# Kernel tuning notes

Measured on AMD Instinct MI355X. Metric: run time of the kernel, lower is better.

## Reference

```python
import jax, jax.numpy as jnp
import numpy as np

M, N, H, C = 32, 1024, 64, 10  # samples, nodes(==feature dim), hidden, classes
SLOPE = 0.2


def setup_inputs() -> dict:
    key = jax.random.key(0)
    ks = jax.random.split(key, 6)
    features = jax.random.normal(ks[0], (M, N, N), jnp.float32)           # [M, N, D], D == N
    weights = jax.random.uniform(ks[1], (M, N, N), jnp.float32)           # nonneg adjacency weights
    std = (2.0 / (1.0 + SLOPE ** 2) / N) ** 0.5                            # kaiming_normal for leaky_relu
    w_gnn0 = jax.random.normal(ks[2], (N, H), jnp.float32) * std
    w_gnn1 = jax.random.normal(ks[3], (N, H), jnp.float32) * std
    w_gnn2 = jax.random.normal(ks[4], (N, H), jnp.float32) * std
    fc_w = jax.random.normal(ks[5], (H, C), jnp.float32) * (1.0 / H ** 0.5)
    fc_b = jnp.zeros((C,), jnp.float32)
    return {
        "features": features,
        "weights": weights,
        "w_gnn0": w_gnn0,
        "w_gnn1": w_gnn1,
        "w_gnn2": w_gnn2,
        "fc_w": fc_w,
        "fc_b": fc_b,
        "view_flag": 0,
    }


def _forward(features, weights, w_gnn0, w_gnn1, w_gnn2, fc_w, fc_b, view_flag):
    Wg = (w_gnn0, w_gnn1, w_gnn2)[view_flag]  # static selection
    _, Nn, _ = features.shape
    Cc = fc_b.shape[0]
    eye = jnp.eye(Nn, dtype=features.dtype)
    rows = jnp.arange(Nn)

    def structural_enhancement(W, p):
        # Literal torch semantics: max_id is always 0 (scores_list[i] is 0-dim),
        # so rows i < p get column-0 entry set to 1 where > 0. Score/cos-sim
        # suppression never affects outputs (scores_list is discarded).
        col0 = W[:, 0]
        new_col0 = jnp.where((rows < p) & (col0 > 0), jnp.asarray(1.0, W.dtype), col0)
        return W.at[:, 0].set(new_col0)

    def per_sample(X, W0):
        XW = X @ Wg  # [N, H]; X and Wg are loop-invariant
        feat_s = jnp.zeros((Wg.shape[1],), X.dtype)
        sr_s = jnp.zeros((Cc,), X.dtype)
        b_s = jnp.zeros((Cc,), X.dtype)
        u_s = jnp.asarray(0.0, X.dtype)
        u0 = jnp.asarray(999.0, X.dtype)
        done = jnp.asarray(False)
        W = W0
        for t in range(1, 9):  # while-loop is bounded: break guaranteed at 5*t >= 40
            adjp = 0.5 * structural_enhancement(W, 5 * t) + eye  # [N, N]
            h = adjp @ XW                                         # [N, H]
            h = jnp.where(h >= 0, h, SLOPE * h)                   # leaky_relu (dropout p=0 / eval)
            feat = h.mean(axis=0)                                 # global avg pool over nodes -> [H]
            sr = jax.nn.softplus(feat @ fc_w + fc_b)              # [C]
            S = sr.sum() + Cc
            u = Cc / S
            brk = (u >= u0) | (5 * t >= 40)
            store = jnp.logical_and(~done, ~brk)
            W = jnp.where(store, adjp, W)
            u0 = jnp.where(store, u, u0)
            feat_s = jnp.where(store, feat, feat_s)
            sr_s = jnp.where(store, sr, sr_s)
            b_s = jnp.where(store, sr / S, b_s)
            u_s = jnp.where(store, u, u_s)
            done = jnp.logical_or(done, brk)
        return feat_s, W, sr_s, b_s, u_s

    return jax.vmap(per_sample)(features, weights)


def reference(features, weights, w_gnn0, w_gnn1, w_gnn2, fc_w, fc_b, view_flag):
    # returns (aft_feat [M,H], weights [M,N,N], single_results [M,C], bb [M,C], uu [M])
    return _forward(features, weights, w_gnn0, w_gnn1, w_gnn2, fc_w, fc_b, view_flag)
```

## Files before the change

kernel.cpp:

```cpp
#include <hip/hip_runtime.h>
#include <math.h>

#define MS 32
#define NN 1024
#define HH 64
#define CC 10
#define SLOPEF 0.2f

typedef __attribute__((ext_vector_type(8))) short bf16x8;
typedef __attribute__((ext_vector_type(4))) float f32x4;
typedef __attribute__((ext_vector_type(4))) unsigned int u32x4;

__device__ __forceinline__ void split2(float v, unsigned short& hi, unsigned short& lo) {
    unsigned u = __builtin_bit_cast(unsigned, v);
    hi = (unsigned short)(u >> 16);
    float hf = __builtin_bit_cast(float, u & 0xFFFF0000u);
    float l = v - hf;
    lo = (unsigned short)(__builtin_bit_cast(unsigned, l) >> 16);
}

__global__ __launch_bounds__(256) void split_B_sel(
    const float* __restrict__ B0, const float* __restrict__ B1,
    const float* __restrict__ B2, const int* __restrict__ flag,
    unsigned short* __restrict__ dh, unsigned short* __restrict__ dl)
{
    int vf = flag[0];
    const float* B = (vf == 0) ? B0 : (vf == 1 ? B1 : B2);
    int c = blockIdx.x;
    const float* src = B + (long)c * 64 * HH;
    unsigned short* dh_img = dh + (long)c * 4096;
    unsigned short* dl_img = dl + (long)c * 4096;

    __shared__ float tile[64][65];
    const int t = threadIdx.x;
    #pragma unroll
    for (int q = 0; q < 4; ++q) {
        int lin = q * 256 + t;
        int r = lin >> 4;
        int c4 = (lin & 15) << 2;
        float4 v = *reinterpret_cast<const float4*>(src + (long)r * HH + c4);
        tile[r][c4 + 0] = v.x; tile[r][c4 + 1] = v.y;
        tile[r][c4 + 2] = v.z; tile[r][c4 + 3] = v.w;
    }
    __syncthreads();
    const int col = t >> 2;
    const int seg = t & 3;
    unsigned short h8[16], l8[16];
    #pragma unroll
    for (int j = 0; j < 16; ++j)
        split2(tile[seg * 16 + j][col], h8[j], l8[j]);
    int base = col * 128 + seg * 32;
    int swz  = (col & 7) << 4;
    *reinterpret_cast<u32x4*>((char*)dh_img + ((base +  0) ^ swz)) = *reinterpret_cast<u32x4*>(h8);
    *reinterpret_cast<u32x4*>((char*)dh_img + ((base + 16) ^ swz)) = *reinterpret_cast<u32x4*>(h8 + 8);
    *reinterpret_cast<u32x4*>((char*)dl_img + ((base +  0) ^ swz)) = *reinterpret_cast<u32x4*>(l8);
    *reinterpret_cast<u32x4*>((char*)dl_img + ((base + 16) ^ swz)) = *reinterpret_cast<u32x4*>(l8 + 8);
}

template <int MODE>
__global__ __launch_bounds__(256, 4) void gemm_split(
    const float* __restrict__ A, long aStride,
    const unsigned short* __restrict__ Bh, const unsigned short* __restrict__ Bl,
    long bStrideH,
    const float* __restrict__ XWf,
    unsigned short* __restrict__ ChOut,
    unsigned short* __restrict__ ClOut,
    float* __restrict__ Cmat)
{
    __shared__ __align__(16) char smem[32768];
    unsigned short* Ahi = (unsigned short*)(smem);
    unsigned short* Alo = (unsigned short*)(smem + 8192);
    unsigned short* Bhi = (unsigned short*)(smem + 16384);
    unsigned short* Blo = (unsigned short*)(smem + 24576);

    const int m = blockIdx.y;
    const int row0 = blockIdx.x * 64;
    const float* A_m = A + (long)m * aStride + (long)row0 * NN;
    const u32x4* bh4 = reinterpret_cast<const u32x4*>(Bh + (bStrideH ? (long)m * bStrideH : 0L));
    const u32x4* bl4 = reinterpret_cast<const u32x4*>(Bl + (bStrideH ? (long)m * bStrideH : 0L));

    const int tid = threadIdx.x;
    const int w   = tid >> 6;
    const int l   = tid & 63;
    const int l15 = l & 15;
    const int lg  = l >> 4;

    f32x4 acc[4] = {};

    int lin_r[4], lin_c4[4];
    #pragma unroll
    for (int q = 0; q < 4; ++q) {
        int lin = q * 256 + tid;
        lin_r[q]  = lin >> 4;
        lin_c4[q] = (lin & 15) << 2;
    }

    f32x4 av[4];
    u32x4 bhreg[2], blreg[2];
    #pragma unroll
    for (int q = 0; q < 4; ++q) {
        const f32x4* p = reinterpret_cast<const f32x4*>(A_m + (long)lin_r[q] * NN + lin_c4[q]);
        av[q] = (MODE == 1) ? *p : __builtin_nontemporal_load(p);
    }
    bhreg[0] = bh4[tid];       bhreg[1] = bh4[256 + tid];
    blreg[0] = bl4[tid];       blreg[1] = bl4[256 + tid];

    for (int kc = 0; kc < 16; ++kc) {
        #pragma unroll
        for (int q = 0; q < 4; ++q) {
            ushort4 h, lw;
            split2(av[q].x, h.x, lw.x);
            split2(av[q].y, h.y, lw.y);
            split2(av[q].z, h.z, lw.z);
            split2(av[q].w, h.w, lw.w);
            int byte = (lin_r[q] * 128 + lin_c4[q] * 2) ^ ((lin_r[q] & 7) << 4);
            *reinterpret_cast<ushort4*>((char*)Ahi + byte) = h;
            *reinterpret_cast<ushort4*>((char*)Alo + byte) = lw;
        }
        reinterpret_cast<u32x4*>(Bhi)[tid]       = bhreg[0];
        reinterpret_cast<u32x4*>(Bhi)[256 + tid] = bhreg[1];
        reinterpret_cast<u32x4*>(Blo)[tid]       = blreg[0];
        reinterpret_cast<u32x4*>(Blo)[256 + tid] = blreg[1];
        __syncthreads();

        if (kc < 15) {
            int ko = (kc + 1) * 64;
            #pragma unroll
            for (int q = 0; q < 4; ++q) {
                const f32x4* p = reinterpret_cast<const f32x4*>(A_m + (long)lin_r[q] * NN + ko + lin_c4[q]);
                av[q] = (MODE == 1) ? *p : __builtin_nontemporal_load(p);
            }
            int cb = (kc + 1) * 512;
            bhreg[0] = bh4[cb + tid];       bhreg[1] = bh4[cb + 256 + tid];
            blreg[0] = bl4[cb + tid];       blreg[1] = bl4[cb + 256 + tid];
        }

        #pragma unroll
        for (int s = 0; s < 2; ++s) {
            int arow  = w * 16 + l15;
            int abyte = (arow * 128 + s * 64 + lg * 16) ^ ((arow & 7) << 4);
            bf16x8 ah = *reinterpret_cast<bf16x8*>((char*)Ahi + abyte);
            bf16x8 al = *reinterpret_cast<bf16x8*>((char*)Alo + abyte);
            #pragma unroll
            for (int fc = 0; fc < 4; ++fc) {
                int col   = fc * 16 + l15;
                int bbyte = (col * 128 + s * 64 + lg * 16) ^ ((col & 7) << 4);
                bf16x8 bh8 = *reinterpret_cast<bf16x8*>((char*)Bhi + bbyte);
                bf16x8 bl8 = *reinterpret_cast<bf16x8*>((char*)Blo + bbyte);
                acc[fc] = __builtin_amdgcn_mfma_f32_16x16x32_bf16(ah, bh8, acc[fc], 0, 0, 0);
                acc[fc] = __builtin_amdgcn_mfma_f32_16x16x32_bf16(ah, bl8, acc[fc], 0, 0, 0);
                acc[fc] = __builtin_amdgcn_mfma_f32_16x16x32_bf16(al, bh8, acc[fc], 0, 0, 0);
            }
        }
        __syncthreads();
    }

    if constexpr (MODE == 0) {
        float* C_m = Cmat + (long)m * NN * HH + (long)row0 * HH;
        unsigned short* dh = ChOut + (long)m * HH * NN + (long)blockIdx.x * 4096;
        unsigned short* dl = ClOut + (long)m * HH * NN + (long)blockIdx.x * 4096;
        const int kb = (w * 16 + lg * 4) * 2;
        #pragma unroll
        for (int fc = 0; fc < 4; ++fc) {
            int col = fc * 16 + l15;
            ushort4 h4, l4;
            split2(acc[fc][0], h4.x, l4.x);
            split2(acc[fc][1], h4.y, l4.y);
            split2(acc[fc][2], h4.z, l4.z);
            split2(acc[fc][3], h4.w, l4.w);
            #pragma unroll
            for (int r = 0; r < 4; ++r) {
                int row = w * 16 + lg * 4 + r;
                C_m[(long)row * HH + col] = acc[fc][r];
            }
            int byte = (col * 128 + kb) ^ ((col & 7) << 4);
            *reinterpret_cast<ushort4*>((char*)dh + byte) = h4;
            *reinterpret_cast<ushort4*>((char*)dl + byte) = l4;
        }
    } else {
        float* red2 = (float*)(smem);
        float* x0s  = (float*)(smem + 8192);
        const float* XWm = XWf + (long)m * NN * HH;
        if (tid < 64) x0s[tid] = XWm[tid];
        __syncthreads();

        int grows[4]; float v[4], bc[4];
        #pragma unroll
        for (int r = 0; r < 4; ++r) {
            int lrow = w * 16 + lg * 4 + r;
            grows[r] = row0 + lrow;
            v[r] = A[(long)m * aStride + (long)grows[r] * NN];
            bc[r] = 0.0f;
        }
        float xwv[4][4];
        #pragma unroll
        for (int fc = 0; fc < 4; ++fc) {
            int col = fc * 16 + l15;
            #pragma unroll
            for (int r = 0; r < 4; ++r)
                xwv[fc][r] = XWm[(long)grows[r] * HH + col];
        }

        float alpha = 1.0f, gamma = 0.0f;
        #pragma unroll
        for (int t = 1; t <= 8; ++t) {
            #pragma unroll
            for (int r = 0; r < 4; ++r) {
                float c = (grows[r] < 5 * t && v[r] > 0.0f) ? (1.0f - v[r]) : 0.0f;
                bc[r] = 0.5f * (bc[r] + c);
                v[r]  = 0.5f * (v[r] + c) + (grows[r] == 0 ? 1.0f : 0.0f);
            }
            alpha *= 0.5f;
            gamma = 0.5f * gamma + 1.0f;
            #pragma unroll
            for (int fc = 0; fc < 4; ++fc) {
                float x0c = x0s[fc * 16 + l15];
                float s = 0.0f;
                #pragma unroll
                for (int r = 0; r < 4; ++r) {
                    float y = alpha * acc[fc][r] + bc[r] * x0c + gamma * xwv[fc][r];
                    s += (y >= 0.0f) ? y : SLOPEF * y;
                }
                s += __shfl_xor(s, 16);
                s += __shfl_xor(s, 32);
                if (l < 16) red2[(w * 8 + (t - 1)) * 64 + fc * 16 + l] = s;
            }
        }
        __syncthreads();
        if (tid < 512) {
            int t8 = tid >> 6, col = tid & 63;
            float p = red2[(0 * 8 + t8) * 64 + col] + red2[(1 * 8 + t8) * 64 + col] +
                      red2[(2 * 8 + t8) * 64 + col] + red2[(3 * 8 + t8) * 64 + col];
            Cmat[(((long)m * 16 + blockIdx.x) * 8 + t8) * 64 + col] = p;
        }
    }
}

__global__ __launch_bounds__(512) void decide_kernel(
    const float* __restrict__ partials,
    const float* __restrict__ weights,
    const float* __restrict__ fc_w,
    const float* __restrict__ fc_b,
    float* __restrict__ col0k,
    int* __restrict__ k_arr,
    float* __restrict__ out_feat,
    float* __restrict__ out_sr,
    float* __restrict__ out_b,
    float* __restrict__ out_u)
{
    __shared__ float feat[8][64];
    __shared__ float sr_all[8][CC];
    __shared__ float Ss[8], us[8];
    __shared__ int ksh;

    const int m = blockIdx.x;
    const int tid = threadIdx.x;

    {
        int t8 = tid >> 6, col = tid & 63;
        float s = 0.0f;
        for (int bx = 0; bx < 16; ++bx)
            s += partials[(((long)m * 16 + bx) * 8 + t8) * 64 + col];
        feat[t8][col] = s * (1.0f / NN);
    }
    __syncthreads();

    if (tid < 80) {
        int t8 = tid / 10, c = tid % 10;
        float a = fc_b[c];
        for (int h = 0; h < HH; ++h) a += feat[t8][h] * fc_w[h * CC + c];
        sr_all[t8][c] = log1pf(expf(-fabsf(a))) + fmaxf(a, 0.0f);
    }
    __syncthreads();

    if (tid < 8) {
        float S = (float)CC;
        for (int c = 0; c < CC; ++c) S += sr_all[tid][c];
        Ss[tid] = S;
        us[tid] = (float)CC / S;
    }
    __syncthreads();

    if (tid == 0) {
        float u0 = 999.0f; int k = 1;
        for (int tt = 1; tt <= 8; ++tt) {
            float u = us[tt - 1];
            int brk = (u >= u0) || (tt == 8);
            if (!brk) { k = tt; u0 = u; } else break;
        }
        ksh = k;
        k_arr[m] = k;
        out_u[m] = us[k - 1];
    }
    __syncthreads();

    const int k = ksh;
    if (tid < 64) out_feat[m * HH + tid] = feat[k - 1][tid];
    if (tid < CC) {
        out_sr[m * CC + tid] = sr_all[k - 1][tid];
        out_b[m * CC + tid]  = sr_all[k - 1][tid] / Ss[k - 1];
    }
    for (int i = tid; i < NN; i += 512) {
        float v = weights[(long)m * NN * NN + (long)i * NN];
        for (int s = 1; s <= k; ++s) {
            float c = (i < 5 * s && v > 0.0f) ? (1.0f - v) : 0.0f;
            v = 0.5f * (v + c) + (i == 0 ? 1.0f : 0.0f);
        }
        col0k[m * NN + i] = v;
    }
}

__global__ __launch_bounds__(256) void finalize_W(
    const float* __restrict__ W0, const float* __restrict__ col0k,
    const int* __restrict__ k_arr, float* __restrict__ outW)
{
    const long n4 = (long)MS * NN * NN / 4;
    const long stride = (long)gridDim.x * 256;
    for (long i4 = (long)blockIdx.x * 256 + threadIdx.x; i4 < n4; i4 += stride) {
        long e = i4 * 4;
        int m = (int)(e >> 20);
        int i = (int)((e >> 10) & 1023);
        int j = (int)(e & 1023);
        int k = k_arr[m];
        float scale = 1.0f / (float)(1 << k);
        float diagadd = 2.0f * (1.0f - scale);

        f32x4 wv = reinterpret_cast<const f32x4*>(W0)[i4];
        float v0 = scale * wv.x + ((i == j + 0) ? diagadd : 0.0f);
        float v1 = scale * wv.y + ((i == j + 1) ? diagadd : 0.0f);
        float v2 = scale * wv.z + ((i == j + 2) ? diagadd : 0.0f);
        float v3 = scale * wv.w + ((i == j + 3) ? diagadd : 0.0f);
        if (j == 0) v0 = col0k[m * NN + i];
        f32x4 o = {v0, v1, v2, v3};
        __builtin_nontemporal_store(o, reinterpret_cast<f32x4*>(outW) + i4);
    }
}

extern "C" void kernel_launch(void* const* d_in, const int* in_sizes, int n_in,
                              void* d_out, int out_size, void* d_ws, size_t ws_size,
                              hipStream_t stream)
{
    const float* features = (const float*)d_in[0];
    const float* weights  = (const float*)d_in[1];
    const float* w_gnn0   = (const float*)d_in[2];
    const float* w_gnn1   = (const float*)d_in[3];
    const float* w_gnn2   = (const float*)d_in[4];
    const float* fc_w     = (const float*)d_in[5];
    const float* fc_b     = (const float*)d_in[6];
    const int*   viewFlag = (const int*)d_in[7];

    float* out = (float*)d_out;
    float* out_feat = out;
    float* outW     = out + (long)MS * HH;
    float* out_sr   = outW + (long)MS * NN * NN;
    float* out_b    = out_sr + MS * CC;
    float* out_u    = out_b + MS * CC;

    float* wsf = (float*)d_ws;
    float* XWf            = wsf;
    unsigned short* XWh   = (unsigned short*)(XWf + (long)MS * NN * HH);
    unsigned short* XWl   = XWh + (long)MS * HH * NN;
    unsigned short* Wgh   = XWl + (long)MS * HH * NN;
    unsigned short* Wgl   = Wgh + (long)HH * NN;
    float* partials       = (float*)(Wgl + (long)HH * NN);
    float* col0k          = partials + (long)MS * 16 * 8 * 64;
    int*   k_arr          = (int*)(col0k + (long)MS * NN);

    split_B_sel<<<16, 256, 0, stream>>>(w_gnn0, w_gnn1, w_gnn2, viewFlag, Wgh, Wgl);
    dim3 gemmGrid(NN / 64, MS);
    gemm_split<0><<<gemmGrid, 256, 0, stream>>>(features, (long)NN * NN,
                                                Wgh, Wgl, 0L, nullptr,
                                                XWh, XWl, XWf);
    gemm_split<1><<<gemmGrid, 256, 0, stream>>>(weights, (long)NN * NN,
                                                XWh, XWl, (long)HH * NN, XWf,
                                                nullptr, nullptr, partials);
    decide_kernel<<<MS, 512, 0, stream>>>(partials, weights, fc_w, fc_b,
                                          col0k, k_arr,
                                          out_feat, out_sr, out_b, out_u);
    finalize_W<<<2048, 256, 0, stream>>>(weights, col0k, k_arr, outW);
}
```

Baseline: 122.0 us.

## Fuse decide step into second GEMM via last-block counter, drop fp32 XW buffer

Moves the per-sample decision logic (feature pooling, classifier, softplus, break selection and column-0 update) into the tail of the second GEMM. The last block to finish for each sample, found through an atomic counter, runs that logic, which removes one kernel launch. The fp32 XW intermediate is no longer written; the second GEMM rebuilds the needed XW values from the bf16 hi/lo split buffers. This saves a 32x1024x64 float store plus its reload, at the cost of slightly different precision for those values and added threadfence/atomic synchronisation.

```diff
diff --git a/kernel.cpp b/kernel.cpp
--- a/kernel.cpp
+++ b/kernel.cpp
@@ -17,6 +17,10 @@
     float hf = __builtin_bit_cast(float, u & 0xFFFF0000u);
     float l = v - hf;
     lo = (unsigned short)(__builtin_bit_cast(unsigned, l) >> 16);
+}
+
+__device__ __forceinline__ float bf16_to_f32(unsigned short h) {
+    return __builtin_bit_cast(float, (unsigned)h << 16);
 }
 
 __global__ __launch_bounds__(256) void split_B_sel(
@@ -62,10 +66,18 @@
     const float* __restrict__ A, long aStride,
     const unsigned short* __restrict__ Bh, const unsigned short* __restrict__ Bl,
     long bStrideH,
-    const float* __restrict__ XWf,
     unsigned short* __restrict__ ChOut,
     unsigned short* __restrict__ ClOut,
-    float* __restrict__ Cmat)
+    float* __restrict__ partials,
+    int* __restrict__ counters,
+    const float* __restrict__ fc_w,
+    const float* __restrict__ fc_b,
+    float* __restrict__ col0k,
+    int* __restrict__ k_arr,
+    float* __restrict__ out_feat,
+    float* __restrict__ out_sr,
+    float* __restrict__ out_b,
+    float* __restrict__ out_u)
 {
     __shared__ __align__(16) char smem[32768];
     unsigned short* Ahi = (unsigned short*)(smem);
@@ -76,14 +88,19 @@
     const int m = blockIdx.y;
     const int row0 = blockIdx.x * 64;
     const float* A_m = A + (long)m * aStride + (long)row0 * NN;
-    const u32x4* bh4 = reinterpret_cast<const u32x4*>(Bh + (bStrideH ? (long)m * bStrideH : 0L));
-    const u32x4* bl4 = reinterpret_cast<const u32x4*>(Bl + (bStrideH ? (long)m * bStrideH : 0L));
+    const unsigned short* bh_us = Bh + (bStrideH ? (long)m * bStrideH : 0L);
+    const unsigned short* bl_us = Bl + (bStrideH ? (long)m * bStrideH : 0L);
+    const u32x4* bh4 = reinterpret_cast<const u32x4*>(bh_us);
+    const u32x4* bl4 = reinterpret_cast<const u32x4*>(bl_us);
 
     const int tid = threadIdx.x;
     const int w   = tid >> 6;
     const int l   = tid & 63;
     const int l15 = l & 15;
     const int lg  = l >> 4;
+
+    if (MODE == 0 && blockIdx.x == 0 && blockIdx.y == 0 && tid < MS)
+        counters[tid] = 0;
 
     f32x4 acc[4] = {};
 
@@ -156,7 +173,6 @@
     }
 
     if constexpr (MODE == 0) {
-        float* C_m = Cmat + (long)m * NN * HH + (long)row0 * HH;
         unsigned short* dh = ChOut + (long)m * HH * NN + (long)blockIdx.x * 4096;
         unsigned short* dl = ClOut + (long)m * HH * NN + (long)blockIdx.x * 4096;
         const int kb = (w * 16 + lg * 4) * 2;
@@ -168,11 +184,6 @@
             split2(acc[fc][1], h4.y, l4.y);
             split2(acc[fc][2], h4.z, l4.z);
             split2(acc[fc][3], h4.w, l4.w);
-            #pragma unroll
-            for (int r = 0; r < 4; ++r) {
-                int row = w * 16 + lg * 4 + r;
-                C_m[(long)row * HH + col] = acc[fc][r];
-            }
             int byte = (col * 128 + kb) ^ ((col & 7) << 4);
             *reinterpret_cast<ushort4*>((char*)dh + byte) = h4;
             *reinterpret_cast<ushort4*>((char*)dl + byte) = l4;
@@ -180,8 +191,12 @@
     } else {
         float* red2 = (float*)(smem);
         float* x0s  = (float*)(smem + 8192);
-        const float* XWm = XWf + (long)m * NN * HH;
-        if (tid < 64) x0s[tid] = XWm[tid];
+        if (tid < 64) {
+            int byte = (tid * 128) ^ ((tid & 7) << 4);
+            float hi = bf16_to_f32(bh_us[byte >> 1]);
+            float lo = bf16_to_f32(bl_us[byte >> 1]);
+            x0s[tid] = hi + lo;
+        }
         __syncthreads();
 
         int grows[4]; float v[4], bc[4];
@@ -197,8 +212,12 @@
         for (int fc = 0; fc < 4; ++fc) {
             int col = fc * 16 + l15;
             #pragma unroll
-            for (int r = 0; r < 4; ++r)
-                xwv[fc][r] = XWm[(long)grows[r] * HH + col];
+            for (int r = 0; r < 4; ++r) {
+                int g = grows[r];
+                long idx = ((long)(g >> 6) * 4096) +
+                           (((col * 128 + (g & 63) * 2) ^ ((col & 7) << 4)) >> 1);
+                xwv[fc][r] = bf16_to_f32(bh_us[idx]) + bf16_to_f32(bl_us[idx]);
+            }
         }
 
         float alpha = 1.0f, gamma = 0.0f;
@@ -231,82 +250,78 @@
             int t8 = tid >> 6, col = tid & 63;
             float p = red2[(0 * 8 + t8) * 64 + col] + red2[(1 * 8 + t8) * 64 + col] +
                       red2[(2 * 8 + t8) * 64 + col] + red2[(3 * 8 + t8) * 64 + col];
-            Cmat[(((long)m * 16 + blockIdx.x) * 8 + t8) * 64 + col] = p;
-        }
-    }
-}
-
-__global__ __launch_bounds__(512) void decide_kernel(
-    const float* __restrict__ partials,
-    const float* __restrict__ weights,
-    const float* __restrict__ fc_w,
-    const float* __restrict__ fc_b,
-    float* __restrict__ col0k,
-    int* __restrict__ k_arr,
-    float* __restrict__ out_feat,
-    float* __restrict__ out_sr,
-    float* __restrict__ out_b,
-    float* __restrict__ out_u)
-{
-    __shared__ float feat[8][64];
-    __shared__ float sr_all[8][CC];
-    __shared__ float Ss[8], us[8];
-    __shared__ int ksh;
-
-    const int m = blockIdx.x;
-    const int tid = threadIdx.x;
-
-    {
-        int t8 = tid >> 6, col = tid & 63;
-        float s = 0.0f;
-        for (int bx = 0; bx < 16; ++bx)
-            s += partials[(((long)m * 16 + bx) * 8 + t8) * 64 + col];
-        feat[t8][col] = s * (1.0f / NN);
-    }
-    __syncthreads();
-
-    if (tid < 80) {
-        int t8 = tid / 10, c = tid % 10;
-        float a = fc_b[c];
-        for (int h = 0; h < HH; ++h) a += feat[t8][h] * fc_w[h * CC + c];
-        sr_all[t8][c] = log1pf(expf(-fabsf(a))) + fmaxf(a, 0.0f);
-    }
-    __syncthreads();
-
-    if (tid < 8) {
-        float S = (float)CC;
-        for (int c = 0; c < CC; ++c) S += sr_all[tid][c];
-        Ss[tid] = S;
-        us[tid] = (float)CC / S;
-    }
-    __syncthreads();
-
-    if (tid == 0) {
-        float u0 = 999.0f; int k = 1;
-        for (int tt = 1; tt <= 8; ++tt) {
-            float u = us[tt - 1];
-            int brk = (u >= u0) || (tt == 8);
-            if (!brk) { k = tt; u0 = u; } else break;
-        }
-        ksh = k;
-        k_arr[m] = k;
-        out_u[m] = us[k - 1];
-    }
-    __syncthreads();
-
-    const int k = ksh;
-    if (tid < 64) out_feat[m * HH + tid] = feat[k - 1][tid];
-    if (tid < CC) {
-        out_sr[m * CC + tid] = sr_all[k - 1][tid];
-        out_b[m * CC + tid]  = sr_all[k - 1][tid] / Ss[k - 1];
-    }
-    for (int i = tid; i < NN; i += 512) {
-        float v = weights[(long)m * NN * NN + (long)i * NN];
-        for (int s = 1; s <= k; ++s) {
-            float c = (i < 5 * s && v > 0.0f) ? (1.0f - v) : 0.0f;
-            v = 0.5f * (v + c) + (i == 0 ? 1.0f : 0.0f);
-        }
-        col0k[m * NN + i] = v;
+            partials[(((long)m * 16 + blockIdx.x) * 8 + t8) * 64 + col] = p;
+        }
+
+        __shared__ int lastFlag;
+        __threadfence();
+        __syncthreads();
+        if (tid == 0) {
+            int old = atomicAdd(&counters[m], 1);
+            lastFlag = (old == 15);
+        }
+        __syncthreads();
+        if (!lastFlag) return;
+        __threadfence();
+
+        float* feat   = (float*)(smem);
+        float* sr_all = (float*)(smem + 2048);
+        float* Ss     = (float*)(smem + 2048 + 8 * CC * 4);
+        float* us     = Ss + 8;
+        int*   kshp   = (int*)(us + 8);
+
+        for (int idx = tid; idx < 512; idx += 256) {
+            int t8 = idx >> 6, col = idx & 63;
+            float s = 0.0f;
+            for (int bx = 0; bx < 16; ++bx)
+                s += partials[(((long)m * 16 + bx) * 8 + t8) * 64 + col];
+            feat[t8 * 64 + col] = s * (1.0f / NN);
+        }
+        __syncthreads();
+
+        if (tid < 80) {
+            int t8 = tid / 10, c = tid % 10;
+            float a = fc_b[c];
+            for (int h = 0; h < HH; ++h) a += feat[t8 * 64 + h] * fc_w[h * CC + c];
+            sr_all[t8 * CC + c] = log1pf(expf(-fabsf(a))) + fmaxf(a, 0.0f);
+        }
+        __syncthreads();
+
+        if (tid < 8) {
+            float S = (float)CC;
+            for (int c = 0; c < CC; ++c) S += sr_all[tid * CC + c];
+            Ss[tid] = S;
+            us[tid] = (float)CC / S;
+        }
+        __syncthreads();
+
+        if (tid == 0) {
+            float u0 = 999.0f; int k = 1;
+            for (int tt = 1; tt <= 8; ++tt) {
+                float u = us[tt - 1];
+                int brk = (u >= u0) || (tt == 8);
+                if (!brk) { k = tt; u0 = u; } else break;
+            }
+            kshp[0] = k;
+            k_arr[m] = k;
+            out_u[m] = us[k - 1];
+        }
+        __syncthreads();
+
+        const int k = kshp[0];
+        if (tid < 64) out_feat[m * HH + tid] = feat[(k - 1) * 64 + tid];
+        if (tid < CC) {
+            out_sr[m * CC + tid] = sr_all[(k - 1) * CC + tid];
+            out_b[m * CC + tid]  = sr_all[(k - 1) * CC + tid] / Ss[k - 1];
+        }
+        for (int i = tid; i < NN; i += 256) {
+            float vv = A[(long)m * aStride + (long)i * NN];
+            for (int s = 1; s <= k; ++s) {
+                float c = (i < 5 * s && vv > 0.0f) ? (1.0f - vv) : 0.0f;
+                vv = 0.5f * (vv + c) + (i == 0 ? 1.0f : 0.0f);
+            }
+            col0k[m * NN + i] = vv;
+        }
     }
 }
 
@@ -356,26 +371,27 @@
     float* out_b    = out_sr + MS * CC;
     float* out_u    = out_b + MS * CC;
 
-    float* wsf = (float*)d_ws;
-    float* XWf            = wsf;
-    unsigned short* XWh   = (unsigned short*)(XWf + (long)MS * NN * HH);
+    char* ws = (char*)d_ws;
+    unsigned short* XWh   = (unsigned short*)ws;
     unsigned short* XWl   = XWh + (long)MS * HH * NN;
     unsigned short* Wgh   = XWl + (long)MS * HH * NN;
     unsigned short* Wgl   = Wgh + (long)HH * NN;
     float* partials       = (float*)(Wgl + (long)HH * NN);
     float* col0k          = partials + (long)MS * 16 * 8 * 64;
     int*   k_arr          = (int*)(col0k + (long)MS * NN);
+    int*   counters       = k_arr + MS;
 
     split_B_sel<<<16, 256, 0, stream>>>(w_gnn0, w_gnn1, w_gnn2, viewFlag, Wgh, Wgl);
     dim3 gemmGrid(NN / 64, MS);
     gemm_split<0><<<gemmGrid, 256, 0, stream>>>(features, (long)NN * NN,
-                                                Wgh, Wgl, 0L, nullptr,
-                                                XWh, XWl, XWf);
+                                                Wgh, Wgl, 0L,
+                                                XWh, XWl, nullptr, counters,
+                                                nullptr, nullptr, nullptr, nullptr,
+                                                nullptr, nullptr, nullptr, nullptr);
     gemm_split<1><<<gemmGrid, 256, 0, stream>>>(weights, (long)NN * NN,
-                                                XWh, XWl, (long)HH * NN, XWf,
-                                                nullptr, nullptr, partials);
-    decide_kernel<<<MS, 512, 0, stream>>>(partials, weights, fc_w, fc_b,
-                                          col0k, k_arr,
-                                          out_feat, out_sr, out_b, out_u);
+                                                XWh, XWl, (long)HH * NN,
+                                                nullptr, nullptr, partials, counters,
+                                                fc_w, fc_b, col0k, k_arr,
+                                                out_feat, out_sr, out_b, out_u);
     finalize_W<<<2048, 256, 0, stream>>>(weights, col0k, k_arr, outW);
 }
```

Result: slower. 158.9 us (+30.2%).
